# Optimization experiments

Measured on AMD Instinct MI355X. Metric: run time of the kernel, lower is better.

The kernel has to match this reference:

```python
import jax, jax.numpy as jnp
import numpy as np

NUM_HEADS = 8
OUT_DIM = 64
HEAD_DIM = OUT_DIM // NUM_HEADS
ALPHA = 0.2  # leaky_relu negative slope


def setup_inputs() -> dict:
    key = jax.random.key(0)
    k1, k2, k3, k4 = jax.random.split(key, 4)
    N, E, IN_DIM = 20000, 4000, 128
    X = jax.random.normal(k1, (N, IN_DIM), dtype=jnp.float32)
    H = jax.random.randint(k2, (N, E), 0, 2, dtype=jnp.int32)  # binary incidence
    # Linear weight (stored [in, out]; equivalent to torch x @ W.T)
    W = jax.random.normal(k3, (IN_DIM, OUT_DIM), dtype=jnp.float32) * (1.0 / np.sqrt(IN_DIM))
    attention = jax.random.normal(k4, (1, NUM_HEADS, 2 * HEAD_DIM), dtype=jnp.float32) * 0.1
    bias = jnp.zeros((OUT_DIM,), dtype=jnp.float32)
    return {"X": X, "H": H, "W": W, "attention": attention, "bias": bias}


def reference(X, H, W, attention, bias):
    N, E = H.shape
    mask = (H > 0).astype(X.dtype)                       # [N, E] membership
    Xh = (X @ W).reshape(N, NUM_HEADS, HEAD_DIM)          # [N, h, d]
    # Original keeps only the self pairwise score: att . concat(x_i, x_i)
    a = attention[0, :, :HEAD_DIM] + attention[0, :, HEAD_DIM:]  # [h, d]
    s = jax.nn.leaky_relu(jnp.einsum('nhd,hd->nh', Xh, a), ALPHA)  # [N, h]
    # Per-hyperedge softmax over member nodes (stable via global per-head max)
    expn = jnp.exp(s - jnp.max(s, axis=0, keepdims=True))          # [N, h]
    denom = jnp.einsum('ne,nh->eh', mask, expn)                    # [E, h]
    weighted = expn[:, :, None] * Xh                               # [N, h, d]
    num = jnp.einsum('ne,nhd->ehd', mask, weighted)                # [E, h, d]
    safe = jnp.where(denom > 0, denom, 1.0)
    agg = jnp.where((denom > 0)[:, :, None], num / safe[:, :, None], 0.0)  # [E, h, d]
    # Scatter the edge aggregate back to every member node
    out = jnp.einsum('ne,ehd->nhd', mask, agg).reshape(N, OUT_DIM) + bias
    return out
```

## Files before the change

### kernel.cpp

```cpp
#include <hip/hip_runtime.h>
#include <math.h>

#define N_NODES 20000
#define N_EDGES 4000
#define IN_DIM 128
#define NUM_HEADS 8
#define ALPHA 0.2f

#define HB_W 64
#define HBT_W 320
#define KPAD1 20480
#define KPAD2 4096
#define IPAD1 4096
#define IPAD2 20224
#define SPLITS1 32
#define SPLITS2 8

typedef float f32x4 __attribute__((ext_vector_type(4)));
typedef __bf16 bf16x8 __attribute__((ext_vector_type(8)));


__device__ __forceinline__ unsigned short f2b(float f) {
    unsigned u = __float_as_uint(f);
    return (unsigned short)((u + 0x7FFFu + ((u >> 16) & 1u)) >> 16);
}

__global__ void __launch_bounds__(256) k_pack(const int* __restrict__ H,
                                              unsigned long long* __restrict__ Hb) {
    __shared__ unsigned char nib[4][64];
    int wq = threadIdx.x >> 6;
    int lane = threadIdx.x & 63;
    int n = blockIdx.x * 4 + wq;
    const int* hrow = H + (size_t)n * N_EDGES;
    unsigned long long* brow = Hb + (size_t)n * HB_W;
    for (int it = 0; it < 16; it++) {
        int e = it * 256 + lane * 4;
        unsigned nb = 0;
        if (e < N_EDGES) {
            int4 v = *(const int4*)(hrow + e);
            nb = (v.x > 0 ? 1u : 0u) | (v.y > 0 ? 2u : 0u) | (v.z > 0 ? 4u : 0u) | (v.w > 0 ? 8u : 0u);
        }
        __syncthreads();
        nib[wq][lane] = (unsigned char)nb;
        __syncthreads();
        if (lane < 16) {
            const unsigned* p = (const unsigned*)&nib[wq][lane * 16];
            unsigned long long w = 0;
#pragma unroll
            for (int c = 0; c < 4; c++) {
                unsigned u = p[c];
                unsigned b16 = (u & 0xFu) | (((u >> 8) & 0xFu) << 4) |
                               (((u >> 16) & 0xFu) << 8) | (((u >> 24) & 0xFu) << 12);
                w |= (unsigned long long)b16 << (16 * c);
            }
            brow[it * 4 + lane] = w;
        }
    }
}

__global__ void __launch_bounds__(256) k_pack2(const int* __restrict__ H,
                                               unsigned long long* __restrict__ Hb) {
    __shared__ unsigned char nib[4][64];
    int wq = threadIdx.x >> 6;
    int lane = threadIdx.x & 63;
    int n = blockIdx.x * 4 + wq;
    const int* hrow = H + (size_t)n * N_EDGES;
    unsigned long long* brow = Hb + (size_t)n * HB_W;
    for (int it = 0; it < 16; it++) {
        int e = it * 256 + lane * 4;
        unsigned nb = 0;
        if (e < N_EDGES) {
            int4 v = *(const int4*)(hrow + e);
            nb = (v.x > 0 ? 1u : 0u) | (v.y > 0 ? 2u : 0u) | (v.z > 0 ? 4u : 0u) | (v.w > 0 ? 8u : 0u);
        }
        __syncthreads();
        nib[wq][lane] = (unsigned char)nb;
        __syncthreads();
        if (lane < 4) {
            const unsigned* p = (const unsigned*)&nib[wq][lane * 16];
            unsigned long long w = 0;
#pragma unroll
            for (int c = 0; c < 4; c++) {
                unsigned u = p[c];
                unsigned b16 = (u & 0xFu) | (((u >> 8) & 0xFu) << 4) |
                               (((u >> 16) & 0xFu) << 8) | (((u >> 24) & 0xFu) << 12);
                w |= (unsigned long long)b16 << (16 * c);
            }
            brow[it * 4 + lane] = w;
        }
    }
}

__global__ void __launch_bounds__(256) k_transB(const unsigned long long* __restrict__ Hb,
                                                unsigned long long* __restrict__ HbT) {
    int wq = threadIdx.x >> 6;
    int lane = threadIdx.x & 63;
    int et = blockIdx.y * 4 + wq;
    if (et >= 63) return;
    int n0 = blockIdx.x * 64;
    int n = n0 + lane;
    unsigned long long w = (n < N_NODES) ? Hb[(size_t)n * HB_W + et] : 0ull;
    unsigned long long out = 0ull;
#pragma unroll
    for (int c = 0; c < 64; c++) {
        unsigned long long b = __ballot((w >> c) & 1ull);
        if (lane == c) out = b;
    }
    int e = et * 64 + lane;
    if (e < N_EDGES) HbT[(size_t)e * HBT_W + blockIdx.x] = out;
}

__global__ void __launch_bounds__(256) k_fused1(const float* __restrict__ X,
                                                const float* __restrict__ W,
                                                const float* __restrict__ att,
                                                float* __restrict__ expn,
                                                float* __restrict__ Yv) {
    int t = blockIdx.x * blockDim.x + threadIdx.x;
    int n = __builtin_amdgcn_readfirstlane(t >> 6);
    int d = t & 63;
    const float* x = X + (size_t)n * IN_DIM;
    float acc = 0.f;
#pragma unroll 8
    for (int k = 0; k < IN_DIM; k++) acc += x[k] * W[k * 64 + d];
    int h = d >> 3, j = d & 7;
    float av = att[h * 16 + j] + att[h * 16 + 8 + j];
    float v = acc * av;
    v += __shfl_xor(v, 1, 64);
    v += __shfl_xor(v, 2, 64);
    v += __shfl_xor(v, 4, 64);
    float s = (v >= 0.f) ? v : ALPHA * v;
    float e = expf(s);
    Yv[(size_t)n * 64 + d] = e * acc;
    if (j == 0) expn[(size_t)n * NUM_HEADS + h] = e;
}

__global__ void __launch_bounds__(256) k_transFE(const float* __restrict__ Yv,
                                                 const float* __restrict__ expn,
                                                 unsigned short* __restrict__ VtT1) {
    __shared__ float tl[64][65];
    int t = threadIdx.x;
    int n0 = blockIdx.x * 64;
    int r = t >> 2, s4 = t & 3;
#pragma unroll
    for (int m = 0; m < 4; m++) {
        int cbase = s4 * 16 + m * 4;
        float4 v = make_float4(0.f, 0.f, 0.f, 0.f);
        if (n0 + r < N_NODES) v = *(const float4*)(Yv + (size_t)(n0 + r) * 64 + cbase);
        tl[r][cbase] = v.x; tl[r][cbase + 1] = v.y; tl[r][cbase + 2] = v.z; tl[r][cbase + 3] = v.w;
    }
    __syncthreads();
    int d = t >> 2;
    unsigned short buf[16];
#pragma unroll
    for (int j = 0; j < 16; j++) buf[j] = f2b(tl[s4 * 16 + j][d]);
    uint4* o = (uint4*)(VtT1 + (size_t)d * KPAD1 + n0 + s4 * 16);
    o[0] = *(uint4*)&buf[0];
    o[1] = *(uint4*)&buf[8];
    int nl = t & 63;
    int rw = t >> 6;
#pragma unroll
    for (int p = 0; p < 4; p++) {
        int row = 64 + rw * 4 + p;
        float v = 0.f;
        if (row < 72 && n0 + nl < N_NODES) v = expn[(size_t)(n0 + nl) * NUM_HEADS + (row - 64)];
        VtT1[(size_t)row * KPAD1 + n0 + nl] = f2b(v);
    }
}

__device__ __forceinline__ bf16x8 expand8(unsigned b) {
    union { uint4 u; bf16x8 v; } cv;
    cv.u.x = ((b & 1u)   ? 0x3F80u : 0u) | ((b & 2u)   ? 0x3F800000u : 0u);
    cv.u.y = ((b & 4u)   ? 0x3F80u : 0u) | ((b & 8u)   ? 0x3F800000u : 0u);
    cv.u.z = ((b & 16u)  ? 0x3F80u : 0u) | ((b & 32u)  ? 0x3F800000u : 0u);
    cv.u.w = ((b & 64u)  ? 0x3F80u : 0u) | ((b & 128u) ? 0x3F800000u : 0u);
    return cv.v;
}
__device__ __forceinline__ bf16x8 ldsread(const unsigned short* p) {
    union { uint4 u; bf16x8 v; } cv;
    cv.u = *(const uint4*)p;
    return cv.v;
}

template <int NCT>
__global__ void __launch_bounds__(256) k_mm(const unsigned long long* __restrict__ bits,
                                            int stride, int I,
                                            const unsigned short* __restrict__ Vg,
                                            int Kpad, int kPerSplit,
                                            float* __restrict__ P, int Ipad) {
    __shared__ __align__(16) unsigned short Vlds[NCT * 16][136];
    const int t = threadIdx.x;
    const int l = t & 63;
    const int w = t >> 6;
    const int q = l >> 4;
    const int cl = l & 15;
    const int rowbase = blockIdx.x * 256 + w * 64;
    const int k0 = blockIdx.y * kPerSplit;
    const int nstages = kPerSplit >> 7;

    const unsigned long long* bp[4];
#pragma unroll
    for (int rt = 0; rt < 4; rt++) {
        int r = rowbase + rt * 16 + cl;
        if (r >= I) r = I - 1;
        bp[rt] = bits + (size_t)r * stride;
    }

    f32x4 acc[4][NCT];
#pragma unroll
    for (int rt = 0; rt < 4; rt++)
#pragma unroll
        for (int c = 0; c < NCT; c++) acc[rt][c] = (f32x4){0.f, 0.f, 0.f, 0.f};

    for (int st = 0; st < nstages; st++) {
        int kc = k0 + st * 128;
        __syncthreads();
#pragma unroll
        for (int ch = t; ch < NCT * 256; ch += 256) {
            int vr = ch >> 4;
            int cj = ch & 15;
            uint4 val = *(const uint4*)(Vg + (size_t)vr * Kpad + kc + cj * 8);
            *(uint4*)&Vlds[vr][cj * 8] = val;
        }
        ulonglong2 wb[4];
#pragma unroll
        for (int rt = 0; rt < 4; rt++) wb[rt] = *(const ulonglong2*)(bp[rt] + (kc >> 6));
        __syncthreads();
#pragma unroll
        for (int kf = 0; kf < 4; kf++) {
            bf16x8 a[4];
#pragma unroll
            for (int rt = 0; rt < 4; rt++) {
                unsigned long long wsel = (kf < 2) ? wb[rt].x : wb[rt].y;
                unsigned byte = (unsigned)(wsel >> ((kf & 1) * 32 + q * 8)) & 0xFFu;
                a[rt] = expand8(byte);
            }
#pragma unroll
            for (int c = 0; c < NCT; c++) {
                bf16x8 bv = ldsread(&Vlds[c * 16 + cl][kf * 32 + q * 8]);
#pragma unroll
                for (int rt = 0; rt < 4; rt++)
                    acc[rt][c] = __builtin_amdgcn_mfma_f32_16x16x32_bf16(a[rt], bv, acc[rt][c], 0, 0, 0);
            }
        }
    }

    size_t base = (size_t)blockIdx.y * Ipad;
#pragma unroll
    for (int rt = 0; rt < 4; rt++)
#pragma unroll
        for (int c = 0; c < NCT; c++)
#pragma unroll
            for (int r = 0; r < 4; r++)
                P[(base + rowbase + rt * 16 + q * 4 + r) * (NCT * 16) + c * 16 + cl] = acc[rt][c][r];
}

__global__ void __launch_bounds__(256) k_aggT(const float* __restrict__ P1,
                                              unsigned short* __restrict__ VtT2) {
    __shared__ float tl[64][65];
    int t = threadIdx.x;
    int e0 = blockIdx.x * 64;
    int el = t >> 2, s4 = t & 3;
    int e = e0 + el;
    float num[16];
#pragma unroll
    for (int j = 0; j < 16; j++) num[j] = 0.f;
    float den0 = 0.f, den1 = 0.f;
    for (int sp = 0; sp < SPLITS1; sp++) {
        const float* row = P1 + ((size_t)sp * IPAD1 + e) * 80;
        const float4* r4 = (const float4*)(row + s4 * 16);
        float4 a = r4[0], b = r4[1], c = r4[2], d = r4[3];
        num[0] += a.x;  num[1] += a.y;  num[2] += a.z;  num[3] += a.w;
        num[4] += b.x;  num[5] += b.y;  num[6] += b.z;  num[7] += b.w;
        num[8] += c.x;  num[9] += c.y;  num[10] += c.z; num[11] += c.w;
        num[12] += d.x; num[13] += d.y; num[14] += d.z; num[15] += d.w;
        float2 dn = *(const float2*)(row + 64 + s4 * 2);
        den0 += dn.x; den1 += dn.y;
    }
#pragma unroll
    for (int j = 0; j < 16; j++) {
        float den = (j < 8) ? den0 : den1;
        float v = (e < N_EDGES && den > 0.f) ? num[j] / den : 0.f;
        tl[el][s4 * 16 + j] = v;
    }
    __syncthreads();
    int d = t >> 2;
    unsigned short buf[16];
#pragma unroll
    for (int j = 0; j < 16; j++) buf[j] = f2b(tl[s4 * 16 + j][d]);
    uint4* o = (uint4*)(VtT2 + (size_t)d * KPAD2 + e0 + s4 * 16);
    o[0] = *(uint4*)&buf[0];
    o[1] = *(uint4*)&buf[8];
}

__global__ void __launch_bounds__(256) k_final(const float* __restrict__ P2,
                                               const float* __restrict__ bias,
                                               float* __restrict__ out) {
    int t = blockIdx.x * blockDim.x + threadIdx.x;
    int n = t >> 6, d = t & 63;
    float v = bias[d];
#pragma unroll
    for (int sp = 0; sp < SPLITS2; sp++) v += P2[((size_t)sp * IPAD2 + n) * 64 + d];
    out[t] = v;
}

extern "C" void kernel_launch(void* const* d_in, const int* in_sizes, int n_in,
                              void* d_out, int out_size, void* d_ws, size_t ws_size,
                              hipStream_t stream) {
    const float* X = (const float*)d_in[0];
    const int* H = (const int*)d_in[1];
    const float* W = (const float*)d_in[2];
    const float* att = (const float*)d_in[3];
    const float* bias = (const float*)d_in[4];
    float* out = (float*)d_out;

    char* ws = (char*)d_ws;
    unsigned long long* Hb  = (unsigned long long*)(ws + 0);
    unsigned long long* HbT = (unsigned long long*)(ws + 10240000);
    unsigned short* VtT1 = (unsigned short*)(ws + 20480000);
    unsigned short* VtT2 = (unsigned short*)(ws + 23756800);
    float* expn = (float*)(ws + 24281088);
    float* Yv   = (float*)(ws + 24921088);
    float* P    = (float*)(ws + 30041088);

    k_pack2<<<5000, 256, 0, stream>>>(H, Hb);
    k_transB<<<dim3(313, 16), 256, 0, stream>>>(Hb, HbT);
    k_fused1<<<5000, 256, 0, stream>>>(X, W, att, expn, Yv);
    k_transFE<<<KPAD1 / 64, 256, 0, stream>>>(Yv, expn, VtT1);
    k_mm<5><<<dim3(IPAD1 / 256, SPLITS1), 256, 0, stream>>>(HbT, HBT_W, N_EDGES, VtT1,
                                                            KPAD1, KPAD1 / SPLITS1, P, IPAD1);
    k_aggT<<<KPAD2 / 64, 256, 0, stream>>>(P, VtT2);
    k_mm<4><<<dim3(IPAD2 / 256, SPLITS2), 256, 0, stream>>>(Hb, HB_W, N_NODES, VtT2,
                                                            KPAD2, KPAD2 / SPLITS2, P, IPAD2);
    k_final<<<5000, 256, 0, stream>>>(P, bias, out);
}
```

Before: 559.0 us.

## Fuse XW projection with transpose, pack bits via shuffles, vectorize final reduce

Merges the projection/score kernel with the bf16 transpose kernel so Yv and expn no longer round-trip through global memory, and each block computes 64 nodes into shared memory before writing the transposed output. The bit-packing kernel replaces its shared-memory nibble staging and barriers with XOR-shuffle OR reductions. The final split-sum kernel switches to float4 loads and stores. Fusing the projection cuts the grid to 320 blocks that each loop over 16 nodes per wave, which may lower parallelism for the projection.

```diff
diff --git a/kernel.cpp b/kernel.cpp
--- a/kernel.cpp
+++ b/kernel.cpp
@@ -25,69 +25,28 @@
     return (unsigned short)((u + 0x7FFFu + ((u >> 16) & 1u)) >> 16);
 }
 
-__global__ void __launch_bounds__(256) k_pack(const int* __restrict__ H,
-                                              unsigned long long* __restrict__ Hb) {
-    __shared__ unsigned char nib[4][64];
+__global__ void __launch_bounds__(256) k_pack4(const int* __restrict__ H,
+                                               unsigned long long* __restrict__ Hb) {
     int wq = threadIdx.x >> 6;
     int lane = threadIdx.x & 63;
     int n = blockIdx.x * 4 + wq;
     const int* hrow = H + (size_t)n * N_EDGES;
     unsigned long long* brow = Hb + (size_t)n * HB_W;
+    int g = lane >> 4;
     for (int it = 0; it < 16; it++) {
         int e = it * 256 + lane * 4;
-        unsigned nb = 0;
+        unsigned long long val = 0ull;
         if (e < N_EDGES) {
             int4 v = *(const int4*)(hrow + e);
-            nb = (v.x > 0 ? 1u : 0u) | (v.y > 0 ? 2u : 0u) | (v.z > 0 ? 4u : 0u) | (v.w > 0 ? 8u : 0u);
+            unsigned nb = (v.x > 0 ? 1u : 0u) | (v.y > 0 ? 2u : 0u) |
+                          (v.z > 0 ? 4u : 0u) | (v.w > 0 ? 8u : 0u);
+            val = (unsigned long long)nb << (4 * (lane & 15));
         }
-        __syncthreads();
-        nib[wq][lane] = (unsigned char)nb;
-        __syncthreads();
-        if (lane < 16) {
-            const unsigned* p = (const unsigned*)&nib[wq][lane * 16];
-            unsigned long long w = 0;
-#pragma unroll
-            for (int c = 0; c < 4; c++) {
-                unsigned u = p[c];
-                unsigned b16 = (u & 0xFu) | (((u >> 8) & 0xFu) << 4) |
-                               (((u >> 16) & 0xFu) << 8) | (((u >> 24) & 0xFu) << 12);
-                w |= (unsigned long long)b16 << (16 * c);
-            }
-            brow[it * 4 + lane] = w;
-        }
-    }
-}
-
-__global__ void __launch_bounds__(256) k_pack2(const int* __restrict__ H,
-                                               unsigned long long* __restrict__ Hb) {
-    __shared__ unsigned char nib[4][64];
-    int wq = threadIdx.x >> 6;
-    int lane = threadIdx.x & 63;
-    int n = blockIdx.x * 4 + wq;
-    const int* hrow = H + (size_t)n * N_EDGES;
-    unsigned long long* brow = Hb + (size_t)n * HB_W;
-    for (int it = 0; it < 16; it++) {
-        int e = it * 256 + lane * 4;
-        unsigned nb = 0;
-        if (e < N_EDGES) {
-            int4 v = *(const int4*)(hrow + e);
-            nb = (v.x > 0 ? 1u : 0u) | (v.y > 0 ? 2u : 0u) | (v.z > 0 ? 4u : 0u) | (v.w > 0 ? 8u : 0u);
-        }
-        __syncthreads();
-        nib[wq][lane] = (unsigned char)nb;
-        __syncthreads();
-        if (lane < 4) {
-            const unsigned* p = (const unsigned*)&nib[wq][lane * 16];
-            unsigned long long w = 0;
-#pragma unroll
-            for (int c = 0; c < 4; c++) {
-                unsigned u = p[c];
-                unsigned b16 = (u & 0xFu) | (((u >> 8) & 0xFu) << 4) |
-                               (((u >> 16) & 0xFu) << 8) | (((u >> 24) & 0xFu) << 12);
-                w |= (unsigned long long)b16 << (16 * c);
-            }
-            brow[it * 4 + lane] = w;
-        }
+        val |= __shfl_xor(val, 1, 64);
+        val |= __shfl_xor(val, 2, 64);
+        val |= __shfl_xor(val, 4, 64);
+        val |= __shfl_xor(val, 8, 64);
+        if ((lane & 15) == 0) brow[it * 4 + g] = val;
     }
 }
 
@@ -110,60 +69,50 @@
     if (e < N_EDGES) HbT[(size_t)e * HBT_W + blockIdx.x] = out;
 }
 
-__global__ void __launch_bounds__(256) k_fused1(const float* __restrict__ X,
+__global__ void __launch_bounds__(256) k_fuseXW(const float* __restrict__ X,
                                                 const float* __restrict__ W,
                                                 const float* __restrict__ att,
-                                                float* __restrict__ expn,
-                                                float* __restrict__ Yv) {
-    int t = blockIdx.x * blockDim.x + threadIdx.x;
-    int n = __builtin_amdgcn_readfirstlane(t >> 6);
-    int d = t & 63;
-    const float* x = X + (size_t)n * IN_DIM;
-    float acc = 0.f;
-#pragma unroll 8
-    for (int k = 0; k < IN_DIM; k++) acc += x[k] * W[k * 64 + d];
+                                                unsigned short* __restrict__ VtT1) {
+    __shared__ float tlY[64][65];
+    __shared__ float tlE[8][72];
+    int t = threadIdx.x;
+    int lane = t & 63;
+    int w = t >> 6;
+    int n0 = blockIdx.x * 64;
+    int d = lane;
     int h = d >> 3, j = d & 7;
     float av = att[h * 16 + j] + att[h * 16 + 8 + j];
-    float v = acc * av;
-    v += __shfl_xor(v, 1, 64);
-    v += __shfl_xor(v, 2, 64);
-    v += __shfl_xor(v, 4, 64);
-    float s = (v >= 0.f) ? v : ALPHA * v;
-    float e = expf(s);
-    Yv[(size_t)n * 64 + d] = e * acc;
-    if (j == 0) expn[(size_t)n * NUM_HEADS + h] = e;
-}
-
-__global__ void __launch_bounds__(256) k_transFE(const float* __restrict__ Yv,
-                                                 const float* __restrict__ expn,
-                                                 unsigned short* __restrict__ VtT1) {
-    __shared__ float tl[64][65];
-    int t = threadIdx.x;
-    int n0 = blockIdx.x * 64;
-    int r = t >> 2, s4 = t & 3;
-#pragma unroll
-    for (int m = 0; m < 4; m++) {
-        int cbase = s4 * 16 + m * 4;
-        float4 v = make_float4(0.f, 0.f, 0.f, 0.f);
-        if (n0 + r < N_NODES) v = *(const float4*)(Yv + (size_t)(n0 + r) * 64 + cbase);
-        tl[r][cbase] = v.x; tl[r][cbase + 1] = v.y; tl[r][cbase + 2] = v.z; tl[r][cbase + 3] = v.w;
+    for (int i = 0; i < 16; i++) {
+        int nl = w * 16 + i;
+        int n = n0 + nl;
+        bool valid = (n < N_NODES);
+        int nc = __builtin_amdgcn_readfirstlane(valid ? n : N_NODES - 1);
+        const float* x = X + (size_t)nc * IN_DIM;
+        float acc = 0.f;
+#pragma unroll 8
+        for (int k = 0; k < IN_DIM; k++) acc += x[k] * W[k * 64 + d];
+        float v = acc * av;
+        v += __shfl_xor(v, 1, 64);
+        v += __shfl_xor(v, 2, 64);
+        v += __shfl_xor(v, 4, 64);
+        float sc = (v >= 0.f) ? v : ALPHA * v;
+        float e = expf(sc);
+        tlY[nl][d] = valid ? e * acc : 0.f;
+        if (j == 0) tlE[h][nl] = valid ? e : 0.f;
     }
     __syncthreads();
-    int d = t >> 2;
+    int dd = t >> 2, s4 = t & 3;
     unsigned short buf[16];
 #pragma unroll
-    for (int j = 0; j < 16; j++) buf[j] = f2b(tl[s4 * 16 + j][d]);
-    uint4* o = (uint4*)(VtT1 + (size_t)d * KPAD1 + n0 + s4 * 16);
+    for (int jj = 0; jj < 16; jj++) buf[jj] = f2b(tlY[s4 * 16 + jj][dd]);
+    uint4* o = (uint4*)(VtT1 + (size_t)dd * KPAD1 + n0 + s4 * 16);
     o[0] = *(uint4*)&buf[0];
     o[1] = *(uint4*)&buf[8];
-    int nl = t & 63;
-    int rw = t >> 6;
 #pragma unroll
     for (int p = 0; p < 4; p++) {
-        int row = 64 + rw * 4 + p;
-        float v = 0.f;
-        if (row < 72 && n0 + nl < N_NODES) v = expn[(size_t)(n0 + nl) * NUM_HEADS + (row - 64)];
-        VtT1[(size_t)row * KPAD1 + n0 + nl] = f2b(v);
+        int row = 64 + w * 4 + p;
+        float v = (row < 72) ? tlE[row - 64][lane] : 0.f;
+        VtT1[(size_t)row * KPAD1 + n0 + lane] = f2b(v);
     }
 }
 
@@ -292,15 +241,18 @@
     o[1] = *(uint4*)&buf[8];
 }
 
-__global__ void __launch_bounds__(256) k_final(const float* __restrict__ P2,
-                                               const float* __restrict__ bias,
-                                               float* __restrict__ out) {
+__global__ void __launch_bounds__(256) k_final4(const float* __restrict__ P2,
+                                                const float* __restrict__ bias,
+                                                float* __restrict__ out) {
     int t = blockIdx.x * blockDim.x + threadIdx.x;
-    int n = t >> 6, d = t & 63;
-    float v = bias[d];
-#pragma unroll
-    for (int sp = 0; sp < SPLITS2; sp++) v += P2[((size_t)sp * IPAD2 + n) * 64 + d];
-    out[t] = v;
+    int n = t >> 4, c4 = t & 15;
+    float4 v = *(const float4*)(bias + c4 * 4);
+#pragma unroll
+    for (int sp = 0; sp < SPLITS2; sp++) {
+        float4 p = *(const float4*)(P2 + ((size_t)sp * IPAD2 + n) * 64 + c4 * 4);
+        v.x += p.x; v.y += p.y; v.z += p.z; v.w += p.w;
+    }
+    *(float4*)(out + (size_t)n * 64 + c4 * 4) = v;
 }
 
 extern "C" void kernel_launch(void* const* d_in, const int* in_sizes, int n_in,
@@ -318,18 +270,15 @@
     unsigned long long* HbT = (unsigned long long*)(ws + 10240000);
     unsigned short* VtT1 = (unsigned short*)(ws + 20480000);
     unsigned short* VtT2 = (unsigned short*)(ws + 23756800);
-    float* expn = (float*)(ws + 24281088);
-    float* Yv   = (float*)(ws + 24921088);
-    float* P    = (float*)(ws + 30041088);
-
-    k_pack2<<<5000, 256, 0, stream>>>(H, Hb);
+    float* P    = (float*)(ws + 24281088);
+
+    k_pack4<<<5000, 256, 0, stream>>>(H, Hb);
     k_transB<<<dim3(313, 16), 256, 0, stream>>>(Hb, HbT);
-    k_fused1<<<5000, 256, 0, stream>>>(X, W, att, expn, Yv);
-    k_transFE<<<KPAD1 / 64, 256, 0, stream>>>(Yv, expn, VtT1);
+    k_fuseXW<<<KPAD1 / 64, 256, 0, stream>>>(X, W, att, VtT1);
     k_mm<5><<<dim3(IPAD1 / 256, SPLITS1), 256, 0, stream>>>(HbT, HBT_W, N_EDGES, VtT1,
                                                             KPAD1, KPAD1 / SPLITS1, P, IPAD1);
     k_aggT<<<KPAD2 / 64, 256, 0, stream>>>(P, VtT2);
     k_mm<4><<<dim3(IPAD2 / 256, SPLITS2), 256, 0, stream>>>(Hb, HB_W, N_NODES, VtT2,
                                                             KPAD2, KPAD2 / SPLITS2, P, IPAD2);
-    k_final<<<5000, 256, 0, stream>>>(P, bias, out);
-}
+    k_final4<<<1250, 256, 0, stream>>>(P, bias, out);
+}
```

Measured after the change: 617.6 us. 1.1x slower.
